# Optimization experiments

Hardware: AMD Instinct MI355X
Metric: run time of the kernel (lower is better)

Reference implementation:

```python
import jax, jax.numpy as jnp
import numpy as np


def setup_inputs() -> dict:
    key = jax.random.key(0)
    k1, k2, k3, k4 = jax.random.split(key, 4)
    B, L, T = 8, 2048, 1024
    Dh, Dg, Dp = 1024, 768, 256
    H = jax.random.normal(k1, (B, L, Dh), dtype=jnp.float32)
    G = jax.random.normal(k2, (B, T, Dg), dtype=jnp.float32)
    # nn.Linear(d_g, d_proj, bias=False).weight -> [d_proj, d_g]
    Wq = jax.random.normal(k3, (Dp, Dg), dtype=jnp.float32) * (Dg ** -0.5)
    Wk = jax.random.normal(k4, (Dp, Dh), dtype=jnp.float32) * (Dh ** -0.5)
    return {"H": H, "G": G, "Wq": Wq, "Wk": Wk}


def reference(H, G, Wq, Wk):
    # GO-token queries attend over protein residues; values are the raw H.
    # The torch module computes this with streaming chunks + online LSE,
    # which is mathematically identical to a single stable softmax attention.
    d_proj = Wq.shape[0]
    scale = d_proj ** -0.5
    Q = jnp.einsum('btg,pg->btp', G, Wq)          # [B,T,Dp]
    K = jnp.einsum('blh,ph->blp', H, Wk)          # [B,L,Dp]
    logits = jnp.einsum('btp,blp->btl', Q, K) * scale  # [B,T,L] fp32
    alpha = jax.nn.softmax(logits, axis=-1)
    # denominator clamp matches torch's s.clamp_min(1e-20) (no-op for unmasked)
    Z = jnp.einsum('btl,blh->bth', alpha, H)      # [B,T,Dh]
    return Z
```

## Files before the change

### kernel.cpp

```cpp
#include <hip/hip_runtime.h>
#include <hip/hip_bf16.h>
#include <type_traits>


typedef float    f32x4  __attribute__((ext_vector_type(4)));
typedef __bf16   bf16x8 __attribute__((ext_vector_type(8)));
typedef unsigned short u16x8 __attribute__((ext_vector_type(8)));

__device__ __forceinline__ unsigned short f2bf(float f) {
    union { float f; unsigned u; } x; x.f = f;
    return (unsigned short)((x.u + 0x7fffu + ((x.u >> 16) & 1u)) >> 16);
}
__device__ __forceinline__ float bf2f(unsigned short u) {
    union { unsigned u; float f; } x; x.u = ((unsigned)u) << 16;
    return x.f;
}
__device__ __forceinline__ void gload_lds16(const unsigned short* g, unsigned short* l) {
    __builtin_amdgcn_global_load_lds(
        (const __attribute__((address_space(1))) void*)g,
        (__attribute__((address_space(3))) void*)l, 16, 0, 0);
}

__global__ __launch_bounds__(256) void kn_transp(const float* __restrict__ H,
                                                 unsigned short* __restrict__ HT,
                                                 int L, int D) {
    __shared__ float tile[32][33];
    int b = blockIdx.z;
    const float* src = H + (size_t)b * L * D;
    unsigned short* dstT = HT + (size_t)b * L * D;
    int l0 = blockIdx.y * 32, d0 = blockIdx.x * 32;
    int tx = threadIdx.x, ty = threadIdx.y;
#pragma unroll
    for (int i = ty; i < 32; i += 8)
        tile[i][tx] = src[(size_t)(l0 + i) * D + d0 + tx];
    __syncthreads();
#pragma unroll
    for (int i = ty; i < 32; i += 8)
        dstT[(size_t)(d0 + i) * L + l0 + tx] = f2bf(tile[tx][i]);
}

template<int TM, int WM>
__device__ __forceinline__ void proj_body(const float* __restrict__ A,
                                          const float* __restrict__ B,
                                          unsigned short* __restrict__ C,
                                          int N, int K, int gxs) {
    constexpr int WN  = 4 / WM;
    constexpr int MF  = (TM / WM) / 16;
    constexpr int NF  = (128 / WN) / 16;
    constexpr int CHA = TM * 8;
    constexpr int CHT = CHA + 1024;
    constexpr int CPT = CHT / 256;
    constexpr int BUFU = TM * 64 + 128 * 64;
    constexpr int LDSB = (2 * BUFU * 2 > TM * 132 * 4) ? 2 * BUFU * 2 : TM * 132 * 4;
    __shared__ __align__(16) char smem_raw[LDSB];
    unsigned short* base = (unsigned short*)smem_raw;
    float* st = (float*)smem_raw;

    int tid = threadIdx.x;
    int t = blockIdx.x;
    int by = t >> gxs;
    int bx = t & ((1 << gxs) - 1);
    const float* Ab = A + (size_t)by * TM * K;
    const float* Bb = B + (size_t)bx * 128 * K;

    int lane = tid & 63;
    int wid = tid >> 6;
    int wr = wid / WN, wc = wid % WN;
    int lr = lane & 15;
    int lg = lane >> 4;
    int xoff = (lane & 7) << 3;

    f32x4 rv[CPT][2];
    f32x4 acc[MF][NF] = {};

    auto LOAD = [&](int k0) {
#pragma unroll
        for (int c = 0; c < CPT; ++c) {
            int ch = c * 256 + tid;
            const float* src;
            if (ch < CHA) {
                int row = ch >> 3;
                src = Ab + (size_t)row * K + k0 + (ch & 7) * 8;
            } else {
                int bc = ch - CHA;
                int row = bc >> 3;
                src = Bb + (size_t)row * K + k0 + (bc & 7) * 8;
            }
            rv[c][0] = *(const f32x4*)src;
            rv[c][1] = *(const f32x4*)(src + 4);
        }
    };
    auto WRITE = [&](int buf) {
        unsigned short* dA = base + buf * BUFU;
        unsigned short* dB = dA + TM * 64;
#pragma unroll
        for (int c = 0; c < CPT; ++c) {
            int ch = c * 256 + tid;
            u16x8 o;
#pragma unroll
            for (int j = 0; j < 4; ++j) { o[j] = f2bf(rv[c][0][j]); o[4 + j] = f2bf(rv[c][1][j]); }
            if (ch < CHA) {
                int row = ch >> 3;
                int sl = (ch & 7) ^ (row & 7);
                *(u16x8*)&dA[row * 64 + sl * 8] = o;
            } else {
                int bc = ch - CHA;
                int row = bc >> 3;
                int sl = (bc & 7) ^ (row & 7);
                *(u16x8*)&dB[row * 64 + sl * 8] = o;
            }
        }
    };
    auto COMPUTE = [&](int buf) {
        unsigned short* pA = base + buf * BUFU;
        unsigned short* pB = pA + TM * 64;
#pragma unroll
        for (int kk = 0; kk < 2; ++kk) {
            int kb = (kk * 32 + lg * 8) ^ xoff;
            bf16x8 af[MF], bfr[NF];
#pragma unroll
            for (int m = 0; m < MF; ++m)
                af[m] = *(const bf16x8*)&pA[(wr * MF * 16 + m * 16 + lr) * 64 + kb];
#pragma unroll
            for (int n = 0; n < NF; ++n)
                bfr[n] = *(const bf16x8*)&pB[(wc * NF * 16 + n * 16 + lr) * 64 + kb];
#pragma unroll
            for (int m = 0; m < MF; ++m)
#pragma unroll
                for (int n = 0; n < NF; ++n)
                    acc[m][n] = __builtin_amdgcn_mfma_f32_16x16x32_bf16(af[m], bfr[n], acc[m][n], 0, 0, 0);
        }
    };

    int nt = K / 64;
    LOAD(0);
    WRITE(0);
    __syncthreads();
    int buf = 0;
    for (int tt = 0; tt < nt; ++tt) {
        if (tt + 1 < nt) LOAD((tt + 1) * 64);
        COMPUTE(buf);
        if (tt + 1 < nt) WRITE(buf ^ 1);
        __syncthreads();
        buf ^= 1;
    }

#pragma unroll
    for (int m = 0; m < MF; ++m) {
        int r0 = wr * MF * 16 + m * 16 + lg * 4;
#pragma unroll
        for (int n = 0; n < NF; ++n) {
            int c0 = wc * NF * 16 + n * 16 + lr;
#pragma unroll
            for (int j = 0; j < 4; ++j)
                st[(r0 + j) * 132 + c0] = acc[m][n][j];
        }
    }
    __syncthreads();
    constexpr int TPR = 256 / TM;
    constexpr int CW  = 128 / TPR;
    int r  = tid / TPR;
    int c0 = (tid % TPR) * CW;
    size_t grow = (size_t)(by * TM + r) * N + bx * 128 + c0;
#pragma unroll
    for (int g = 0; g < CW / 8; ++g) {
        f32x4 a = *(const f32x4*)&st[r * 132 + c0 + g * 8];
        f32x4 b = *(const f32x4*)&st[r * 132 + c0 + g * 8 + 4];
        u16x8 o;
#pragma unroll
        for (int j = 0; j < 4; ++j) { o[j] = f2bf(a[j]); o[4 + j] = f2bf(b[j]); }
        *(u16x8*)&C[grow + g * 8] = o;
    }
}

__global__ __launch_bounds__(256) void kn_qproj(const float* A, const float* B,
                                                unsigned short* C, int N, int K, int gxs) {
    proj_body<32, 1>(A, B, C, N, K, gxs);
}
__global__ __launch_bounds__(256) void kn_kproj(const float* A, const float* B,
                                                unsigned short* C, int N, int K, int gxs) {
    proj_body<64, 2>(A, B, C, N, K, gxs);
}

__global__ __launch_bounds__(512) void kn_sgemm(const unsigned short* __restrict__ A,
                                                const unsigned short* __restrict__ B,
                                                unsigned short* __restrict__ C,
                                                float* __restrict__ rowsum,
                                                int N, int K, int Trows,
                                                long batchA, long batchB, long batchC,
                                                float scale, int gxs) {
    __shared__ __align__(16) char smem_raw[49152];
    unsigned short* base = (unsigned short*)smem_raw;
    float* st = (float*)smem_raw;

    int tid = threadIdx.x;
    int wg = blockIdx.x;
    int bz = wg & 7;
    int t = wg >> 3;
    int by = t >> gxs;
    int bx = t & ((1 << gxs) - 1);

    const unsigned short* Ab = A + (size_t)bz * batchA + (size_t)by * 256 * K;
    const unsigned short* Bb = B + (size_t)bz * batchB + (size_t)bx * 128 * K;
    unsigned short* Cb = C + (size_t)bz * batchC;
    float* rs = rowsum + (size_t)bz * Trows;

    int lane = tid & 63;
    int wid = tid >> 6;
    int wr = wid >> 1, wc = wid & 1;
    int lr = lane & 15;
    int lg = lane >> 4;
    int xoff = (lane & 7) << 3;

    f32x4 acc[4][4] = {};

    for (int k0 = 0; k0 < K; k0 += 64) {
#pragma unroll
        for (int c = 0; c < 6; ++c) {
            int ch = c * 512 + tid;
            if (ch < 2048) {
                int row = ch >> 3;
                int g8 = (ch & 7) ^ (row & 7);
                gload_lds16(Ab + (size_t)row * K + k0 + g8 * 8, base + ch * 8);
            } else {
                int bc = ch - 2048;
                int row = bc >> 3;
                int g8 = (bc & 7) ^ (row & 7);
                gload_lds16(Bb + (size_t)row * K + k0 + g8 * 8, base + 16384 + bc * 8);
            }
        }
        __syncthreads();
#pragma unroll
        for (int kk = 0; kk < 2; ++kk) {
            int kb = (kk * 32 + lg * 8) ^ xoff;
            bf16x8 af[4], bfr[4];
#pragma unroll
            for (int m = 0; m < 4; ++m)
                af[m] = *(const bf16x8*)&base[(wr * 64 + m * 16 + lr) * 64 + kb];
#pragma unroll
            for (int n = 0; n < 4; ++n)
                bfr[n] = *(const bf16x8*)&base[16384 + (wc * 64 + n * 16 + lr) * 64 + kb];
#pragma unroll
            for (int m = 0; m < 4; ++m)
#pragma unroll
                for (int n = 0; n < 4; ++n)
                    acc[m][n] = __builtin_amdgcn_mfma_f32_16x16x32_bf16(af[m], bfr[n], acc[m][n], 0, 0, 0);
        }
        __syncthreads();
    }

#pragma unroll
    for (int q = 0; q < 4; ++q) {
        if (wr == q) {
#pragma unroll
            for (int m = 0; m < 4; ++m) {
                int rl = m * 16 + lg * 4;
#pragma unroll
                for (int n = 0; n < 4; ++n) {
                    int col = wc * 64 + n * 16 + lr;
#pragma unroll
                    for (int j = 0; j < 4; ++j)
                        st[(rl + j) * 132 + col] = acc[m][n][j] * scale;
                }
            }
        }
        __syncthreads();
        int r = tid >> 3;
        int c0 = (tid & 7) * 16;
        size_t grow = (size_t)(by * 256 + q * 64 + r) * N + bx * 128 + c0;
        float psum = 0.f;
#pragma unroll
        for (int g = 0; g < 2; ++g) {
            f32x4 a = *(const f32x4*)&st[r * 132 + c0 + g * 8];
            f32x4 b = *(const f32x4*)&st[r * 132 + c0 + g * 8 + 4];
            u16x8 o;
#pragma unroll
            for (int j = 0; j < 4; ++j) {
                float pa = __expf(a[j]);
                float pb = __expf(b[j]);
                o[j] = f2bf(pa); o[4 + j] = f2bf(pb);
                psum += bf2f(o[j]) + bf2f(o[4 + j]);
            }
            *(u16x8*)&Cb[grow + g * 8] = o;
        }
        psum += __shfl_xor(psum, 1);
        psum += __shfl_xor(psum, 2);
        psum += __shfl_xor(psum, 4);
        if ((tid & 7) == 0)
            atomicAdd(&rs[by * 256 + q * 64 + r], psum);
        __syncthreads();
    }
}

__global__ __launch_bounds__(512) void kn_pv(const unsigned short* __restrict__ A,
                                             const unsigned short* __restrict__ B,
                                             float* __restrict__ C,
                                             const float* __restrict__ rowsum,
                                             int N, int K, int Trows,
                                             long batchA, long batchB, long batchC,
                                             int gxs) {
    __shared__ __align__(16) char smem_raw[3 * 49152];
    unsigned short* base = (unsigned short*)smem_raw;
    float* st = (float*)smem_raw;

    int tid = threadIdx.x;
    int wg = blockIdx.x;
    int bz = wg & 7;
    int t = wg >> 3;
    int by = t >> gxs;
    int bx = t & ((1 << gxs) - 1);

    const unsigned short* Ab = A + (size_t)bz * batchA + (size_t)by * 256 * K;
    const unsigned short* Bb = B + (size_t)bz * batchB + (size_t)bx * 128 * K;
    float* Cb = C + (size_t)bz * batchC;
    const float* rs = rowsum + (size_t)bz * Trows;

    int lane = tid & 63;
    int wid = tid >> 6;
    int wr = wid >> 1, wc = wid & 1;
    int lr = lane & 15;
    int lg = lane >> 4;
    int xoff = (lane & 7) << 3;

    f32x4 acc[4][4] = {};
    bf16x8 fA0[4], fB0[4], fA1[4], fB1[4];

    auto STAGE_HALF = [&](int buf, int k0, int half) {
        unsigned short* dA = base + buf * 24576;
        unsigned short* dB = dA + 16384;
#pragma unroll
        for (int c = 0; c < 3; ++c) {
            int ch = half * 1536 + c * 512 + tid;
            if (ch < 2048) {
                int row = ch >> 3;
                int g8 = (ch & 7) ^ (row & 7);
                gload_lds16(Ab + (size_t)row * K + k0 + g8 * 8, dA + ch * 8);
            } else {
                int bc = ch - 2048;
                int row = bc >> 3;
                int g8 = (bc & 7) ^ (row & 7);
                gload_lds16(Bb + (size_t)row * K + k0 + g8 * 8, dB + bc * 8);
            }
        }
    };
    auto LDFRAG = [&](int buf, int kk, bf16x8* fa, bf16x8* fb) {
        unsigned short* pA = base + buf * 24576;
        unsigned short* pB = pA + 16384;
        int kb = (kk * 32 + lg * 8) ^ xoff;
#pragma unroll
        for (int m = 0; m < 4; ++m)
            fa[m] = *(const bf16x8*)&pA[(wr * 64 + m * 16 + lr) * 64 + kb];
#pragma unroll
        for (int n = 0; n < 4; ++n)
            fb[n] = *(const bf16x8*)&pB[(wc * 64 + n * 16 + lr) * 64 + kb];
    };

    int nt = K / 64;
    STAGE_HALF(0, 0, 0);   STAGE_HALF(0, 0, 1);
    STAGE_HALF(1, 64, 0);  STAGE_HALF(1, 64, 1);
    asm volatile("s_waitcnt vmcnt(6)" ::: "memory");
    __builtin_amdgcn_s_barrier();
    LDFRAG(0, 0, fA0, fB0);

    int cur = 0;
    for (int tt = 0; tt < nt; ++tt) {
        int nb  = (cur >= 1) ? cur - 1 : 2;
        int nxt = (cur == 2) ? 0 : cur + 1;
        if (tt + 2 < nt) STAGE_HALF(nb, (tt + 2) * 64, 0);
        LDFRAG(cur, 1, fA1, fB1);
        __builtin_amdgcn_sched_barrier(0);
        __builtin_amdgcn_s_setprio(1);
#pragma unroll
        for (int m = 0; m < 4; ++m)
#pragma unroll
            for (int n = 0; n < 4; ++n)
                acc[m][n] = __builtin_amdgcn_mfma_f32_16x16x32_bf16(fA0[m], fB0[n], acc[m][n], 0, 0, 0);
        __builtin_amdgcn_s_setprio(0);
        __builtin_amdgcn_sched_barrier(0);
        if (tt + 2 < nt) STAGE_HALF(nb, (tt + 2) * 64, 1);
        __builtin_amdgcn_sched_barrier(0);
        __builtin_amdgcn_s_setprio(1);
#pragma unroll
        for (int m = 0; m < 4; ++m)
#pragma unroll
            for (int n = 0; n < 4; ++n)
                acc[m][n] = __builtin_amdgcn_mfma_f32_16x16x32_bf16(fA1[m], fB1[n], acc[m][n], 0, 0, 0);
        __builtin_amdgcn_s_setprio(0);
        __builtin_amdgcn_sched_barrier(0);
        if (tt + 1 < nt) {
            if (tt + 2 < nt) asm volatile("s_waitcnt vmcnt(6)" ::: "memory");
            else             asm volatile("s_waitcnt vmcnt(0)" ::: "memory");
            LDFRAG(nxt, 0, fA0, fB0);
            __builtin_amdgcn_sched_barrier(0);
            __builtin_amdgcn_s_barrier();
        }
        cur = nxt;
    }
    __syncthreads();

#pragma unroll
    for (int q = 0; q < 4; ++q) {
        if (wr == q) {
#pragma unroll
            for (int m = 0; m < 4; ++m) {
                int rl = m * 16 + lg * 4;
#pragma unroll
                for (int n = 0; n < 4; ++n) {
                    int col = wc * 64 + n * 16 + lr;
#pragma unroll
                    for (int j = 0; j < 4; ++j)
                        st[(rl + j) * 132 + col] = acc[m][n][j];
                }
            }
        }
        __syncthreads();
        int r = tid >> 3;
        int c0 = (tid & 7) * 16;
        float inv = 1.0f / rs[by * 256 + q * 64 + r];
        size_t grow = (size_t)(by * 256 + q * 64 + r) * N + bx * 128 + c0;
#pragma unroll
        for (int g = 0; g < 4; ++g) {
            f32x4 v = *(const f32x4*)&st[r * 132 + c0 + g * 4];
#pragma unroll
            for (int j = 0; j < 4; ++j) v[j] *= inv;
            *(f32x4*)&Cb[grow + g * 4] = v;
        }
        __syncthreads();
    }
}

extern "C" void kernel_launch(void* const* d_in, const int* in_sizes, int n_in,
                              void* d_out, int out_size, void* d_ws, size_t ws_size,
                              hipStream_t stream) {
    constexpr int B = 8, L = 2048, T = 1024, Dh = 1024, Dg = 768, Dp = 256;
    const float* H  = (const float*)d_in[0];
    const float* G  = (const float*)d_in[1];
    const float* Wq = (const float*)d_in[2];
    const float* Wk = (const float*)d_in[3];
    float* Z = (float*)d_out;

    unsigned short* Qbf = (unsigned short*)d_ws;
    unsigned short* Kbf = Qbf + (size_t)B * T * Dp;
    unsigned short* HT  = Kbf + (size_t)B * L * Dp;
    unsigned short* S   = HT  + (size_t)B * Dh * L;
    float* rowsum = (float*)(S + (size_t)B * T * L);

    hipMemsetAsync(rowsum, 0, (size_t)B * T * sizeof(float), stream);

    kn_transp<<<dim3(Dh / 32, L / 32, B), dim3(32, 8), 0, stream>>>(H, HT, L, Dh);

    kn_qproj<<<(B * T / 32) * (Dp / 128), 256, 0, stream>>>(G, Wq, Qbf, Dp, Dg, 1);

    kn_kproj<<<(B * L / 64) * (Dp / 128), 256, 0, stream>>>(H, Wk, Kbf, Dp, Dh, 1);

    kn_sgemm<<<(T / 256) * (L / 128) * B, 512, 0, stream>>>
        (Qbf, Kbf, S, rowsum, L, Dp, T, (long)T * Dp, (long)L * Dp, (long)T * L, 0.0625f, 4);

    kn_pv<<<(T / 256) * (Dh / 128) * B, 512, 0, stream>>>
        (S, HT, Z, rowsum, Dh, L, T, (long)T * L, (long)Dh * L, (long)T * Dh, 3);
}
```

Measured before the change: 147.5 us.

## Shrink GEMM tiles to 128x128 with simple K=32 loop, drop pipelining and LDS epilogue

The score and PV GEMMs now use 128x128 output tiles with a plain single-buffer K-step of 32. This replaces the 256-row tiles, the XOR-swizzled LDS, the triple-buffered prefetch and the LDS-staged coalesced epilogue. Outputs are written straight from MFMA accumulators with scattered stores, and row sums are reduced with shuffles. The transpose kernel moves to 64x64 tiles. Smaller tiles mean more blocks and less LDS per block, but they give up the latency hiding, the bank-conflict avoidance and the coalesced stores, and they reload more data from global memory.

Result: slower. 153.8 us (+4.2%).

```diff
diff --git a/kernel.cpp b/kernel.cpp
--- a/kernel.cpp
+++ b/kernel.cpp
@@ -24,18 +24,18 @@
 __global__ __launch_bounds__(256) void kn_transp(const float* __restrict__ H,
                                                  unsigned short* __restrict__ HT,
                                                  int L, int D) {
-    __shared__ float tile[32][33];
+    __shared__ float tile[64][65];
     int b = blockIdx.z;
     const float* src = H + (size_t)b * L * D;
     unsigned short* dstT = HT + (size_t)b * L * D;
-    int l0 = blockIdx.y * 32, d0 = blockIdx.x * 32;
+    int l0 = blockIdx.y * 64, d0 = blockIdx.x * 64;
     int tx = threadIdx.x, ty = threadIdx.y;
 #pragma unroll
-    for (int i = ty; i < 32; i += 8)
+    for (int i = ty; i < 64; i += 4)
         tile[i][tx] = src[(size_t)(l0 + i) * D + d0 + tx];
     __syncthreads();
 #pragma unroll
-    for (int i = ty; i < 32; i += 8)
+    for (int i = ty; i < 64; i += 4)
         dstT[(size_t)(d0 + i) * L + l0 + tx] = f2bf(tile[tx][i]);
 }
 
@@ -182,6 +182,24 @@
     proj_body<64, 2>(A, B, C, N, K, gxs);
 }
 
+
+__device__ __forceinline__ void stage128(const unsigned short* Ab, const unsigned short* Bb,
+                                         int K, int k0, unsigned short* sA, unsigned short* sB,
+                                         int tid) {
+#pragma unroll
+    for (int c = 0; c < 2; ++c) {
+        int ch = c * 512 + tid;
+        if (ch < 512) {
+            int row = ch >> 2;
+            gload_lds16(Ab + (size_t)row * K + k0 + (ch & 3) * 8, sA + ch * 8);
+        } else {
+            int bc = ch - 512;
+            int row = bc >> 2;
+            gload_lds16(Bb + (size_t)row * K + k0 + (bc & 3) * 8, sB + bc * 8);
+        }
+    }
+}
+
 __global__ __launch_bounds__(512) void kn_sgemm(const unsigned short* __restrict__ A,
                                                 const unsigned short* __restrict__ B,
                                                 unsigned short* __restrict__ C,
@@ -189,9 +207,8 @@
                                                 int N, int K, int Trows,
                                                 long batchA, long batchB, long batchC,
                                                 float scale, int gxs) {
-    __shared__ __align__(16) char smem_raw[49152];
-    unsigned short* base = (unsigned short*)smem_raw;
-    float* st = (float*)smem_raw;
+    __shared__ __align__(16) unsigned short sA[128 * 32];
+    __shared__ __align__(16) unsigned short sB[128 * 32];
 
     int tid = threadIdx.x;
     int wg = blockIdx.x;
@@ -200,7 +217,7 @@
     int by = t >> gxs;
     int bx = t & ((1 << gxs) - 1);
 
-    const unsigned short* Ab = A + (size_t)bz * batchA + (size_t)by * 256 * K;
+    const unsigned short* Ab = A + (size_t)bz * batchA + (size_t)by * 128 * K;
     const unsigned short* Bb = B + (size_t)bz * batchB + (size_t)bx * 128 * K;
     unsigned short* Cb = C + (size_t)bz * batchC;
     float* rs = rowsum + (size_t)bz * Trows;
@@ -210,86 +227,54 @@
     int wr = wid >> 1, wc = wid & 1;
     int lr = lane & 15;
     int lg = lane >> 4;
-    int xoff = (lane & 7) << 3;
-
-    f32x4 acc[4][4] = {};
-
-    for (int k0 = 0; k0 < K; k0 += 64) {
-#pragma unroll
-        for (int c = 0; c < 6; ++c) {
-            int ch = c * 512 + tid;
-            if (ch < 2048) {
-                int row = ch >> 3;
-                int g8 = (ch & 7) ^ (row & 7);
-                gload_lds16(Ab + (size_t)row * K + k0 + g8 * 8, base + ch * 8);
-            } else {
-                int bc = ch - 2048;
-                int row = bc >> 3;
-                int g8 = (bc & 7) ^ (row & 7);
-                gload_lds16(Bb + (size_t)row * K + k0 + g8 * 8, base + 16384 + bc * 8);
+
+    f32x4 acc[2][4] = {};
+
+    for (int k0 = 0; k0 < K; k0 += 32) {
+        stage128(Ab, Bb, K, k0, sA, sB, tid);
+        __syncthreads();
+        bf16x8 af[2], bfr[4];
+#pragma unroll
+        for (int m = 0; m < 2; ++m)
+            af[m] = *(const bf16x8*)&sA[(wr * 32 + m * 16 + lr) * 32 + lg * 8];
+#pragma unroll
+        for (int n = 0; n < 4; ++n)
+            bfr[n] = *(const bf16x8*)&sB[(wc * 64 + n * 16 + lr) * 32 + lg * 8];
+#pragma unroll
+        for (int m = 0; m < 2; ++m)
+#pragma unroll
+            for (int n = 0; n < 4; ++n)
+                acc[m][n] = __builtin_amdgcn_mfma_f32_16x16x32_bf16(af[m], bfr[n], acc[m][n], 0, 0, 0);
+        __syncthreads();
+    }
+
+    float psum[2][4] = {};
+#pragma unroll
+    for (int m = 0; m < 2; ++m) {
+#pragma unroll
+        for (int j = 0; j < 4; ++j) {
+            int row = by * 128 + wr * 32 + m * 16 + lg * 4 + j;
+#pragma unroll
+            for (int n = 0; n < 4; ++n) {
+                int col = bx * 128 + wc * 64 + n * 16 + lr;
+                unsigned short ov = f2bf(__expf(acc[m][n][j] * scale));
+                Cb[(size_t)row * N + col] = ov;
+                psum[m][j] += bf2f(ov);
             }
         }
-        __syncthreads();
-#pragma unroll
-        for (int kk = 0; kk < 2; ++kk) {
-            int kb = (kk * 32 + lg * 8) ^ xoff;
-            bf16x8 af[4], bfr[4];
-#pragma unroll
-            for (int m = 0; m < 4; ++m)
-                af[m] = *(const bf16x8*)&base[(wr * 64 + m * 16 + lr) * 64 + kb];
-#pragma unroll
-            for (int n = 0; n < 4; ++n)
-                bfr[n] = *(const bf16x8*)&base[16384 + (wc * 64 + n * 16 + lr) * 64 + kb];
-#pragma unroll
-            for (int m = 0; m < 4; ++m)
-#pragma unroll
-                for (int n = 0; n < 4; ++n)
-                    acc[m][n] = __builtin_amdgcn_mfma_f32_16x16x32_bf16(af[m], bfr[n], acc[m][n], 0, 0, 0);
-        }
-        __syncthreads();
-    }
-
-#pragma unroll
-    for (int q = 0; q < 4; ++q) {
-        if (wr == q) {
-#pragma unroll
-            for (int m = 0; m < 4; ++m) {
-                int rl = m * 16 + lg * 4;
-#pragma unroll
-                for (int n = 0; n < 4; ++n) {
-                    int col = wc * 64 + n * 16 + lr;
-#pragma unroll
-                    for (int j = 0; j < 4; ++j)
-                        st[(rl + j) * 132 + col] = acc[m][n][j] * scale;
-                }
-            }
-        }
-        __syncthreads();
-        int r = tid >> 3;
-        int c0 = (tid & 7) * 16;
-        size_t grow = (size_t)(by * 256 + q * 64 + r) * N + bx * 128 + c0;
-        float psum = 0.f;
-#pragma unroll
-        for (int g = 0; g < 2; ++g) {
-            f32x4 a = *(const f32x4*)&st[r * 132 + c0 + g * 8];
-            f32x4 b = *(const f32x4*)&st[r * 132 + c0 + g * 8 + 4];
-            u16x8 o;
-#pragma unroll
-            for (int j = 0; j < 4; ++j) {
-                float pa = __expf(a[j]);
-                float pb = __expf(b[j]);
-                o[j] = f2bf(pa); o[4 + j] = f2bf(pb);
-                psum += bf2f(o[j]) + bf2f(o[4 + j]);
-            }
-            *(u16x8*)&Cb[grow + g * 8] = o;
-        }
-        psum += __shfl_xor(psum, 1);
-        psum += __shfl_xor(psum, 2);
-        psum += __shfl_xor(psum, 4);
-        if ((tid & 7) == 0)
-            atomicAdd(&rs[by * 256 + q * 64 + r], psum);
-        __syncthreads();
-    }
+    }
+#pragma unroll
+    for (int m = 0; m < 2; ++m)
+#pragma unroll
+        for (int j = 0; j < 4; ++j) {
+            float s = psum[m][j];
+            s += __shfl_xor(s, 1);
+            s += __shfl_xor(s, 2);
+            s += __shfl_xor(s, 4);
+            s += __shfl_xor(s, 8);
+            if (lr == 0)
+                atomicAdd(&rs[by * 128 + wr * 32 + m * 16 + lg * 4 + j], s);
+        }
 }
 
 __global__ __launch_bounds__(512) void kn_pv(const unsigned short* __restrict__ A,
@@ -299,9 +284,8 @@
                                              int N, int K, int Trows,
                                              long batchA, long batchB, long batchC,
                                              int gxs) {
-    __shared__ __align__(16) char smem_raw[3 * 49152];
-    unsigned short* base = (unsigned short*)smem_raw;
-    float* st = (float*)smem_raw;
+    __shared__ __align__(16) unsigned short sA[128 * 32];
+    __shared__ __align__(16) unsigned short sB[128 * 32];
 
     int tid = threadIdx.x;
     int wg = blockIdx.x;
@@ -310,7 +294,7 @@
     int by = t >> gxs;
     int bx = t & ((1 << gxs) - 1);
 
-    const unsigned short* Ab = A + (size_t)bz * batchA + (size_t)by * 256 * K;
+    const unsigned short* Ab = A + (size_t)bz * batchA + (size_t)by * 128 * K;
     const unsigned short* Bb = B + (size_t)bz * batchB + (size_t)bx * 128 * K;
     float* Cb = C + (size_t)bz * batchC;
     const float* rs = rowsum + (size_t)bz * Trows;
@@ -320,112 +304,39 @@
     int wr = wid >> 1, wc = wid & 1;
     int lr = lane & 15;
     int lg = lane >> 4;
-    int xoff = (lane & 7) << 3;
-
-    f32x4 acc[4][4] = {};
-    bf16x8 fA0[4], fB0[4], fA1[4], fB1[4];
-
-    auto STAGE_HALF = [&](int buf, int k0, int half) {
-        unsigned short* dA = base + buf * 24576;
-        unsigned short* dB = dA + 16384;
-#pragma unroll
-        for (int c = 0; c < 3; ++c) {
-            int ch = half * 1536 + c * 512 + tid;
-            if (ch < 2048) {
-                int row = ch >> 3;
-                int g8 = (ch & 7) ^ (row & 7);
-                gload_lds16(Ab + (size_t)row * K + k0 + g8 * 8, dA + ch * 8);
-            } else {
-                int bc = ch - 2048;
-                int row = bc >> 3;
-                int g8 = (bc & 7) ^ (row & 7);
-                gload_lds16(Bb + (size_t)row * K + k0 + g8 * 8, dB + bc * 8);
+
+    f32x4 acc[2][4] = {};
+
+    for (int k0 = 0; k0 < K; k0 += 32) {
+        stage128(Ab, Bb, K, k0, sA, sB, tid);
+        __syncthreads();
+        bf16x8 af[2], bfr[4];
+#pragma unroll
+        for (int m = 0; m < 2; ++m)
+            af[m] = *(const bf16x8*)&sA[(wr * 32 + m * 16 + lr) * 32 + lg * 8];
+#pragma unroll
+        for (int n = 0; n < 4; ++n)
+            bfr[n] = *(const bf16x8*)&sB[(wc * 64 + n * 16 + lr) * 32 + lg * 8];
+#pragma unroll
+        for (int m = 0; m < 2; ++m)
+#pragma unroll
+            for (int n = 0; n < 4; ++n)
+                acc[m][n] = __builtin_amdgcn_mfma_f32_16x16x32_bf16(af[m], bfr[n], acc[m][n], 0, 0, 0);
+        __syncthreads();
+    }
+
+#pragma unroll
+    for (int m = 0; m < 2; ++m) {
+#pragma unroll
+        for (int j = 0; j < 4; ++j) {
+            int rloc = by * 128 + wr * 32 + m * 16 + lg * 4 + j;
+            float inv = 1.0f / rs[rloc];
+#pragma unroll
+            for (int n = 0; n < 4; ++n) {
+                int col = bx * 128 + wc * 64 + n * 16 + lr;
+                Cb[(size_t)rloc * N + col] = acc[m][n][j] * inv;
             }
         }
-    };
-    auto LDFRAG = [&](int buf, int kk, bf16x8* fa, bf16x8* fb) {
-        unsigned short* pA = base + buf * 24576;
-        unsigned short* pB = pA + 16384;
-        int kb = (kk * 32 + lg * 8) ^ xoff;
-#pragma unroll
-        for (int m = 0; m < 4; ++m)
-            fa[m] = *(const bf16x8*)&pA[(wr * 64 + m * 16 + lr) * 64 + kb];
-#pragma unroll
-        for (int n = 0; n < 4; ++n)
-            fb[n] = *(const bf16x8*)&pB[(wc * 64 + n * 16 + lr) * 64 + kb];
-    };
-
-    int nt = K / 64;
-    STAGE_HALF(0, 0, 0);   STAGE_HALF(0, 0, 1);
-    STAGE_HALF(1, 64, 0);  STAGE_HALF(1, 64, 1);
-    asm volatile("s_waitcnt vmcnt(6)" ::: "memory");
-    __builtin_amdgcn_s_barrier();
-    LDFRAG(0, 0, fA0, fB0);
-
-    int cur = 0;
-    for (int tt = 0; tt < nt; ++tt) {
-        int nb  = (cur >= 1) ? cur - 1 : 2;
-        int nxt = (cur == 2) ? 0 : cur + 1;
-        if (tt + 2 < nt) STAGE_HALF(nb, (tt + 2) * 64, 0);
-        LDFRAG(cur, 1, fA1, fB1);
-        __builtin_amdgcn_sched_barrier(0);
-        __builtin_amdgcn_s_setprio(1);
-#pragma unroll
-        for (int m = 0; m < 4; ++m)
-#pragma unroll
-            for (int n = 0; n < 4; ++n)
-                acc[m][n] = __builtin_amdgcn_mfma_f32_16x16x32_bf16(fA0[m], fB0[n], acc[m][n], 0, 0, 0);
-        __builtin_amdgcn_s_setprio(0);
-        __builtin_amdgcn_sched_barrier(0);
-        if (tt + 2 < nt) STAGE_HALF(nb, (tt + 2) * 64, 1);
-        __builtin_amdgcn_sched_barrier(0);
-        __builtin_amdgcn_s_setprio(1);
-#pragma unroll
-        for (int m = 0; m < 4; ++m)
-#pragma unroll
-            for (int n = 0; n < 4; ++n)
-                acc[m][n] = __builtin_amdgcn_mfma_f32_16x16x32_bf16(fA1[m], fB1[n], acc[m][n], 0, 0, 0);
-        __builtin_amdgcn_s_setprio(0);
-        __builtin_amdgcn_sched_barrier(0);
-        if (tt + 1 < nt) {
-            if (tt + 2 < nt) asm volatile("s_waitcnt vmcnt(6)" ::: "memory");
-            else             asm volatile("s_waitcnt vmcnt(0)" ::: "memory");
-            LDFRAG(nxt, 0, fA0, fB0);
-            __builtin_amdgcn_sched_barrier(0);
-            __builtin_amdgcn_s_barrier();
-        }
-        cur = nxt;
-    }
-    __syncthreads();
-
-#pragma unroll
-    for (int q = 0; q < 4; ++q) {
-        if (wr == q) {
-#pragma unroll
-            for (int m = 0; m < 4; ++m) {
-                int rl = m * 16 + lg * 4;
-#pragma unroll
-                for (int n = 0; n < 4; ++n) {
-                    int col = wc * 64 + n * 16 + lr;
-#pragma unroll
-                    for (int j = 0; j < 4; ++j)
-                        st[(rl + j) * 132 + col] = acc[m][n][j];
-                }
-            }
-        }
-        __syncthreads();
-        int r = tid >> 3;
-        int c0 = (tid & 7) * 16;
-        float inv = 1.0f / rs[by * 256 + q * 64 + r];
-        size_t grow = (size_t)(by * 256 + q * 64 + r) * N + bx * 128 + c0;
-#pragma unroll
-        for (int g = 0; g < 4; ++g) {
-            f32x4 v = *(const f32x4*)&st[r * 132 + c0 + g * 4];
-#pragma unroll
-            for (int j = 0; j < 4; ++j) v[j] *= inv;
-            *(f32x4*)&Cb[grow + g * 4] = v;
-        }
-        __syncthreads();
     }
 }
 
@@ -447,15 +358,15 @@
 
     hipMemsetAsync(rowsum, 0, (size_t)B * T * sizeof(float), stream);
 
-    kn_transp<<<dim3(Dh / 32, L / 32, B), dim3(32, 8), 0, stream>>>(H, HT, L, Dh);
+    kn_transp<<<dim3(Dh / 64, L / 64, B), dim3(64, 4), 0, stream>>>(H, HT, L, Dh);
 
     kn_qproj<<<(B * T / 32) * (Dp / 128), 256, 0, stream>>>(G, Wq, Qbf, Dp, Dg, 1);
 
     kn_kproj<<<(B * L / 64) * (Dp / 128), 256, 0, stream>>>(H, Wk, Kbf, Dp, Dh, 1);
 
-    kn_sgemm<<<(T / 256) * (L / 128) * B, 512, 0, stream>>>
+    kn_sgemm<<<(T / 128) * (L / 128) * B, 512, 0, stream>>>
         (Qbf, Kbf, S, rowsum, L, Dp, T, (long)T * Dp, (long)L * Dp, (long)T * L, 0.0625f, 4);
 
-    kn_pv<<<(T / 256) * (Dh / 128) * B, 512, 0, stream>>>
+    kn_pv<<<(T / 128) * (Dh / 128) * B, 512, 0, stream>>>
         (S, HT, Z, rowsum, Dh, L, T, (long)T * L, (long)Dh * L, (long)T * Dh, 3);
 }
```

## Deepen PV pipeline to 6-stage K=32 ring, widen transpose tiles, use native bf16 convert

Applied to the files above, without the earlier changes.

The PV GEMM drops its 3-buffer K=64 half-staged pipeline with register double-buffered fragments. In its place is a 6-deep ring of K=32 LDS buffers with 5 tiles in flight, one barrier per tile and an XOR swizzle adapted to 4 chunks per row. The H transpose kernel now uses 64x64 tiles with 64x4 threads, and f2bf uses the hardware bf16 conversion. The aim is to hide more global latency in the dominant GEMM, but the change adds a barrier per 32-wide K step and removes the overlap of fragment loads with MFMA.

Result: no change. 148.2 us (+0.5%).

```diff
diff --git a/kernel.cpp b/kernel.cpp
--- a/kernel.cpp
+++ b/kernel.cpp
@@ -8,8 +8,9 @@
 typedef unsigned short u16x8 __attribute__((ext_vector_type(8)));
 
 __device__ __forceinline__ unsigned short f2bf(float f) {
-    union { float f; unsigned u; } x; x.f = f;
-    return (unsigned short)((x.u + 0x7fffu + ((x.u >> 16) & 1u)) >> 16);
+    union { __bf16 b; unsigned short u; } c;
+    c.b = (__bf16)f;
+    return c.u;
 }
 __device__ __forceinline__ float bf2f(unsigned short u) {
     union { unsigned u; float f; } x; x.u = ((unsigned)u) << 16;
@@ -24,18 +25,18 @@
 __global__ __launch_bounds__(256) void kn_transp(const float* __restrict__ H,
                                                  unsigned short* __restrict__ HT,
                                                  int L, int D) {
-    __shared__ float tile[32][33];
+    __shared__ float tile[64][65];
     int b = blockIdx.z;
     const float* src = H + (size_t)b * L * D;
     unsigned short* dstT = HT + (size_t)b * L * D;
-    int l0 = blockIdx.y * 32, d0 = blockIdx.x * 32;
+    int l0 = blockIdx.y * 64, d0 = blockIdx.x * 64;
     int tx = threadIdx.x, ty = threadIdx.y;
 #pragma unroll
-    for (int i = ty; i < 32; i += 8)
+    for (int i = ty; i < 64; i += 4)
         tile[i][tx] = src[(size_t)(l0 + i) * D + d0 + tx];
     __syncthreads();
 #pragma unroll
-    for (int i = ty; i < 32; i += 8)
+    for (int i = ty; i < 64; i += 4)
         dstT[(size_t)(d0 + i) * L + l0 + tx] = f2bf(tile[tx][i]);
 }
 
@@ -267,7 +268,8 @@
         __syncthreads();
         int r = tid >> 3;
         int c0 = (tid & 7) * 16;
-        size_t grow = (size_t)(by * 256 + q * 64 + r) * N + bx * 128 + c0;
+        int grow_r = by * 256 + q * 64 + r;
+        size_t grow = (size_t)grow_r * N + bx * 128 + c0;
         float psum = 0.f;
 #pragma unroll
         for (int g = 0; g < 2; ++g) {
@@ -276,9 +278,8 @@
             u16x8 o;
 #pragma unroll
             for (int j = 0; j < 4; ++j) {
-                float pa = __expf(a[j]);
-                float pb = __expf(b[j]);
-                o[j] = f2bf(pa); o[4 + j] = f2bf(pb);
+                o[j]     = f2bf(__expf(a[j]));
+                o[4 + j] = f2bf(__expf(b[j]));
                 psum += bf2f(o[j]) + bf2f(o[4 + j]);
             }
             *(u16x8*)&Cb[grow + g * 8] = o;
@@ -287,7 +288,7 @@
         psum += __shfl_xor(psum, 2);
         psum += __shfl_xor(psum, 4);
         if ((tid & 7) == 0)
-            atomicAdd(&rs[by * 256 + q * 64 + r], psum);
+            atomicAdd(&rs[grow_r], psum);
         __syncthreads();
     }
 }
@@ -299,9 +300,9 @@
                                              int N, int K, int Trows,
                                              long batchA, long batchB, long batchC,
                                              int gxs) {
-    __shared__ __align__(16) char smem_raw[3 * 49152];
-    unsigned short* base = (unsigned short*)smem_raw;
-    float* st = (float*)smem_raw;
+    constexpr int BUFU = 256 * 32 + 128 * 32;
+    __shared__ __align__(16) unsigned short smem[6 * BUFU];
+    float* st = (float*)smem;
 
     int tid = threadIdx.x;
     int wg = blockIdx.x;
@@ -320,81 +321,63 @@
     int wr = wid >> 1, wc = wid & 1;
     int lr = lane & 15;
     int lg = lane >> 4;
-    int xoff = (lane & 7) << 3;
 
     f32x4 acc[4][4] = {};
-    bf16x8 fA0[4], fB0[4], fA1[4], fB1[4];
-
-    auto STAGE_HALF = [&](int buf, int k0, int half) {
-        unsigned short* dA = base + buf * 24576;
-        unsigned short* dB = dA + 16384;
+
+    auto STAGE = [&](int buf, int k0) {
+        unsigned short* dA = smem + buf * BUFU;
+        unsigned short* dB = dA + 8192;
 #pragma unroll
         for (int c = 0; c < 3; ++c) {
-            int ch = half * 1536 + c * 512 + tid;
-            if (ch < 2048) {
-                int row = ch >> 3;
-                int g8 = (ch & 7) ^ (row & 7);
-                gload_lds16(Ab + (size_t)row * K + k0 + g8 * 8, dA + ch * 8);
+            int ch = c * 512 + tid;
+            if (ch < 1024) {
+                int row = ch >> 2;
+                int g4 = (ch & 3) ^ (row & 3);
+                gload_lds16(Ab + (size_t)row * K + k0 + g4 * 8, dA + ch * 8);
             } else {
-                int bc = ch - 2048;
-                int row = bc >> 3;
-                int g8 = (bc & 7) ^ (row & 7);
-                gload_lds16(Bb + (size_t)row * K + k0 + g8 * 8, dB + bc * 8);
+                int bc = ch - 1024;
+                int row = bc >> 2;
+                int g4 = (bc & 3) ^ (row & 3);
+                gload_lds16(Bb + (size_t)row * K + k0 + g4 * 8, dB + bc * 8);
             }
         }
     };
-    auto LDFRAG = [&](int buf, int kk, bf16x8* fa, bf16x8* fb) {
-        unsigned short* pA = base + buf * 24576;
-        unsigned short* pB = pA + 16384;
-        int kb = (kk * 32 + lg * 8) ^ xoff;
+
+    int nt = K / 32;
+    STAGE(0, 0); STAGE(1, 32); STAGE(2, 64); STAGE(3, 96); STAGE(4, 128);
+
+    int ka = (lg ^ (lr & 3)) * 8;
+
+    for (int tt = 0; tt < nt; ++tt) {
+        int rem = nt - 1 - tt;
+        if (rem >= 5)      asm volatile("s_waitcnt vmcnt(15)" ::: "memory");
+        else if (rem == 4) asm volatile("s_waitcnt vmcnt(12)" ::: "memory");
+        else if (rem == 3) asm volatile("s_waitcnt vmcnt(9)" ::: "memory");
+        else if (rem == 2) asm volatile("s_waitcnt vmcnt(6)" ::: "memory");
+        else if (rem == 1) asm volatile("s_waitcnt vmcnt(3)" ::: "memory");
+        else               asm volatile("s_waitcnt vmcnt(0)" ::: "memory");
+        __builtin_amdgcn_s_barrier();
+
+        unsigned short* pA = smem + (tt % 6) * BUFU;
+        unsigned short* pB = pA + 8192;
+        bf16x8 fa[4], fb[4];
 #pragma unroll
         for (int m = 0; m < 4; ++m)
-            fa[m] = *(const bf16x8*)&pA[(wr * 64 + m * 16 + lr) * 64 + kb];
+            fa[m] = *(const bf16x8*)&pA[(wr * 64 + m * 16 + lr) * 32 + ka];
 #pragma unroll
         for (int n = 0; n < 4; ++n)
-            fb[n] = *(const bf16x8*)&pB[(wc * 64 + n * 16 + lr) * 64 + kb];
-    };
-
-    int nt = K / 64;
-    STAGE_HALF(0, 0, 0);   STAGE_HALF(0, 0, 1);
-    STAGE_HALF(1, 64, 0);  STAGE_HALF(1, 64, 1);
-    asm volatile("s_waitcnt vmcnt(6)" ::: "memory");
-    __builtin_amdgcn_s_barrier();
-    LDFRAG(0, 0, fA0, fB0);
-
-    int cur = 0;
-    for (int tt = 0; tt < nt; ++tt) {
-        int nb  = (cur >= 1) ? cur - 1 : 2;
-        int nxt = (cur == 2) ? 0 : cur + 1;
-        if (tt + 2 < nt) STAGE_HALF(nb, (tt + 2) * 64, 0);
-        LDFRAG(cur, 1, fA1, fB1);
+            fb[n] = *(const bf16x8*)&pB[(wc * 64 + n * 16 + lr) * 32 + ka];
+
+        if (tt + 5 < nt) STAGE((tt + 5) % 6, (tt + 5) * 32);
         __builtin_amdgcn_sched_barrier(0);
+
         __builtin_amdgcn_s_setprio(1);
 #pragma unroll
         for (int m = 0; m < 4; ++m)
 #pragma unroll
             for (int n = 0; n < 4; ++n)
-                acc[m][n] = __builtin_amdgcn_mfma_f32_16x16x32_bf16(fA0[m], fB0[n], acc[m][n], 0, 0, 0);
+                acc[m][n] = __builtin_amdgcn_mfma_f32_16x16x32_bf16(fa[m], fb[n], acc[m][n], 0, 0, 0);
         __builtin_amdgcn_s_setprio(0);
-        __builtin_amdgcn_sched_barrier(0);
-        if (tt + 2 < nt) STAGE_HALF(nb, (tt + 2) * 64, 1);
-        __builtin_amdgcn_sched_barrier(0);
-        __builtin_amdgcn_s_setprio(1);
-#pragma unroll
-        for (int m = 0; m < 4; ++m)
-#pragma unroll
-            for (int n = 0; n < 4; ++n)
-                acc[m][n] = __builtin_amdgcn_mfma_f32_16x16x32_bf16(fA1[m], fB1[n], acc[m][n], 0, 0, 0);
-        __builtin_amdgcn_s_setprio(0);
-        __builtin_amdgcn_sched_barrier(0);
-        if (tt + 1 < nt) {
-            if (tt + 2 < nt) asm volatile("s_waitcnt vmcnt(6)" ::: "memory");
-            else             asm volatile("s_waitcnt vmcnt(0)" ::: "memory");
-            LDFRAG(nxt, 0, fA0, fB0);
-            __builtin_amdgcn_sched_barrier(0);
-            __builtin_amdgcn_s_barrier();
-        }
-        cur = nxt;
     }
     __syncthreads();
 
@@ -447,7 +430,7 @@
 
     hipMemsetAsync(rowsum, 0, (size_t)B * T * sizeof(float), stream);
 
-    kn_transp<<<dim3(Dh / 32, L / 32, B), dim3(32, 8), 0, stream>>>(H, HT, L, Dh);
+    kn_transp<<<dim3(Dh / 64, L / 64, B), dim3(64, 4), 0, stream>>>(H, HT, L, Dh);
 
     kn_qproj<<<(B * T / 32) * (Dp / 128), 256, 0, stream>>>(G, Wq, Qbf, Dp, Dg, 1);
 
```
